# Optimization experiments

Hardware: AMD Instinct MI355X
Metric: run time of the kernel (lower is better)

Reference implementation:

```python
import jax, jax.numpy as jnp
import numpy as np


def setup_inputs() -> dict:
    key = jax.random.key(0)
    k1, k2, k3, k4 = jax.random.split(key, 4)
    B, S, d_in, d_out = 4, 2048, 1024, 1024
    x = jax.random.normal(k1, (B, S, d_in), dtype=jnp.float32)
    # torch nn.Linear weight is [d_out, d_in]; we store transposed [d_in, d_out]
    Wq = jax.random.normal(k2, (d_in, d_out), dtype=jnp.float32) * (1.0 / np.sqrt(d_in))
    Wk = jax.random.normal(k3, (d_in, d_out), dtype=jnp.float32) * (1.0 / np.sqrt(d_in))
    Wv = jax.random.normal(k4, (d_in, d_out), dtype=jnp.float32) * (1.0 / np.sqrt(d_in))
    return {"x": x, "Wq": Wq, "Wk": Wk, "Wv": Wv}


def reference(x, Wq, Wk, Wv):
    # x: [B, S, d_in]
    B, S, d_in = x.shape
    q = jnp.einsum("bsd,de->bse", x, Wq)
    k = jnp.einsum("bsd,de->bse", x, Wk)
    v = jnp.einsum("bsd,de->bse", x, Wv)
    scores = jnp.einsum("bqe,bke->bqk", q, k)  # [B, S, S]
    causal = jnp.triu(jnp.ones((S, S), dtype=bool), k=1)  # True above diagonal
    scores = jnp.where(causal[None, :, :], -jnp.inf, scores)
    # NOTE: original scales by sqrt(d_in), not sqrt(d_out)
    scale = jnp.asarray(1.0 / np.sqrt(d_in), dtype=scores.dtype)
    weights = jax.nn.softmax(scores * scale, axis=-1)
    # dropout p=0.0 -> identity
    return jnp.einsum("bqk,bke->bqe", weights, v)
```

## Files before the change

kernel.cpp:

```cpp
#include <hip/hip_runtime.h>
#include <hip/hip_bf16.h>

typedef __attribute__((ext_vector_type(8))) short short8;
typedef __attribute__((ext_vector_type(4))) short short4_t;
typedef __attribute__((ext_vector_type(4))) float f32x4;
typedef unsigned short ushort_t;

__device__ __forceinline__ ushort_t f2bf(float f) {
    union { __hip_bfloat16 h; ushort_t u; } c;
    c.h = __float2bfloat16(f);
    return c.u;
}

__device__ __forceinline__ void gload16(const ushort_t* g, ushort_t* l) {
    __builtin_amdgcn_global_load_lds(
        (const __attribute__((address_space(1))) void*)g,
        (__attribute__((address_space(3))) void*)l, 16, 0, 0);
}

__global__ __launch_bounds__(256) void k_prep(const float* __restrict__ x,
                                              const float* __restrict__ Wq,
                                              const float* __restrict__ Wk,
                                              const float* __restrict__ Wv,
                                              ushort_t* __restrict__ xb,
                                              ushort_t* __restrict__ Wqb,
                                              ushort_t* __restrict__ Wkb,
                                              ushort_t* __restrict__ Wvt) {
    const int bz = blockIdx.z;
    const int t = threadIdx.y * 32 + threadIdx.x;
    if (bz == 3) {
        size_t base = ((size_t)(blockIdx.y * 32 + blockIdx.x) * 256 + t) * 8;
#pragma unroll
        for (int p = 0; p < 4; ++p) {
            size_t idx = base + (size_t)p * 2097152;
            float4 a = *(const float4*)(x + idx);
            float4 b = *(const float4*)(x + idx + 4);
            short8 o;
            o[0] = (short)f2bf(a.x); o[1] = (short)f2bf(a.y);
            o[2] = (short)f2bf(a.z); o[3] = (short)f2bf(a.w);
            o[4] = (short)f2bf(b.x); o[5] = (short)f2bf(b.y);
            o[6] = (short)f2bf(b.z); o[7] = (short)f2bf(b.w);
            *(short8*)(xb + idx) = o;
        }
        return;
    }
    if (bz < 2) {
        const float* src = bz ? Wk : Wq;
        ushort_t* dst = bz ? Wkb : Wqb;
        size_t idx = ((size_t)(blockIdx.y * 32 + blockIdx.x) * 256 + t) * 4;
        float4 a = *(const float4*)(src + idx);
        short4_t o;
        o[0] = (short)f2bf(a.x); o[1] = (short)f2bf(a.y);
        o[2] = (short)f2bf(a.z); o[3] = (short)f2bf(a.w);
        *(short4_t*)(dst + idx) = o;
        return;
    }
    __shared__ float tile[32][33];
    int tx = threadIdx.x, ty = threadIdx.y;
    int d0 = blockIdx.y * 32, e0 = blockIdx.x * 32;
#pragma unroll
    for (int i = 0; i < 32; i += 8)
        tile[ty + i][tx] = Wv[(size_t)(d0 + ty + i) * 1024 + e0 + tx];
    __syncthreads();
#pragma unroll
    for (int i = 0; i < 32; i += 8)
        Wvt[(size_t)(e0 + ty + i) * 1024 + d0 + tx] = f2bf(tile[tx][ty + i]);
}

template <int MODE>
__global__ __launch_bounds__(256) void k_gemm(const ushort_t* __restrict__ Abase,
                                              const ushort_t* __restrict__ Bbase,
                                              void* __restrict__ Cbase,
                                              ushort_t* __restrict__ Vt) {
    int bm, bn, bz;
    const ushort_t* A;
    const ushort_t* B;
    if constexpr (MODE == 3) {
        bm = blockIdx.x; bn = blockIdx.y; bz = 0;
        A = Abase; B = Bbase;
    } else {
        bm = blockIdx.x; bn = blockIdx.y; bz = blockIdx.z;
        A = Abase;
        B = Bbase + (size_t)bz * 1048576;
    }
    const int lda = 1024, ldb = 1024, nk = 32;

    constexpr int SMEM_ELEMS = (MODE == 0) ? (128 * 130) : 8192;
    __shared__ ushort_t smem[SMEM_ELEMS];
    ushort_t* As = smem;
    ushort_t* Bs = smem + 4096;

    const int tid = threadIdx.x;
    const int l = tid & 63, wid = tid >> 6;
    const int wr = (wid >> 1) * 64, wc = (wid & 1) * 64;
    const int lr = l & 15, kc = (l >> 4) * 8;

    const int srow = tid >> 2, skb = (tid & 3) * 8;
    const ushort_t* ag = A + (size_t)(bm * 128 + srow) * lda + skb;
    const ushort_t* bg = B + (size_t)(bn * 128 + srow) * ldb + skb;
    const size_t a64 = (size_t)64 * lda, b64 = (size_t)64 * ldb;
    ushort_t* al = As + tid * 8;
    ushort_t* bl = Bs + tid * 8;

    f32x4 zero = {0.f, 0.f, 0.f, 0.f};
    f32x4 acc[4][4];
#pragma unroll
    for (int m = 0; m < 4; ++m)
#pragma unroll
        for (int n = 0; n < 4; ++n) acc[m][n] = zero;

    for (int ks = 0; ks < nk; ++ks) {
        __syncthreads();
        gload16(ag, al);
        gload16(ag + a64, al + 2048);
        gload16(bg, bl);
        gload16(bg + b64, bl + 2048);
        ag += 32; bg += 32;
        __syncthreads();

        short8 a[4], b[4];
#pragma unroll
        for (int m = 0; m < 4; ++m)
            a[m] = *(const short8*)&As[(wr + m * 16 + lr) * 32 + kc];
#pragma unroll
        for (int n = 0; n < 4; ++n)
            b[n] = *(const short8*)&Bs[(wc + n * 16 + lr) * 32 + kc];
#pragma unroll
        for (int m = 0; m < 4; ++m)
#pragma unroll
            for (int n = 0; n < 4; ++n)
                acc[m][n] = __builtin_amdgcn_mfma_f32_16x16x32_bf16(a[m], b[n], acc[m][n], 0, 0, 0);
    }

    const int rbase = (l >> 4) * 4;
    const int cbase = l & 15;

    if constexpr (MODE == 0) {
        if (bz == 1) {
            __syncthreads();
#pragma unroll
            for (int m = 0; m < 4; ++m)
#pragma unroll
                for (int n = 0; n < 4; ++n) {
                    int col = wc + n * 16 + cbase;
                    int row0 = wr + m * 16 + rbase;
#pragma unroll
                    for (int r = 0; r < 4; ++r)
                        smem[col * 130 + row0 + r] = f2bf(acc[m][n][r]);
                }
            __syncthreads();
            const int e = tid >> 1, jh = (tid & 1) * 64;
            const int b = bm >> 4, j0 = (bm * 128) & 2047;
            ushort_t* dst = Vt + (size_t)b * 2097152 +
                            (size_t)(bn * 128 + e) * 2048 + j0 + jh;
            const ushort_t* src = smem + e * 130 + jh;
#pragma unroll
            for (int c = 0; c < 8; ++c)
                *(short8*)(dst + c * 8) = *(const short8*)(src + c * 8);
            return;
        }
    }

#pragma unroll
    for (int m = 0; m < 4; ++m) {
#pragma unroll
        for (int n = 0; n < 4; ++n) {
            int col = wc + n * 16 + cbase;
            int gcol = bn * 128 + col;
#pragma unroll
            for (int r = 0; r < 4; ++r) {
                int grow = bm * 128 + wr + m * 16 + rbase + r;
                ushort_t* C = (ushort_t*)Cbase;
                C[(size_t)grow * 1024 + gcol] = f2bf(acc[m][n][r]);
            }
        }
    }
}

template <int MODE>
__global__ __launch_bounds__(256) void k_attn(const ushort_t* __restrict__ Abase,
                                              const ushort_t* __restrict__ Bbase,
                                              void* __restrict__ Cbase) {
    int bm, bn;
    const int bz = blockIdx.z;
    const ushort_t* A;
    const ushort_t* B;
    int lda, ldb, nk;
    if constexpr (MODE == 1) {
        int x = blockIdx.x;
        bm = (int)((sqrtf(8.f * x + 1.f) - 1.f) * 0.5f);
        while ((bm + 1) * (bm + 2) / 2 <= x) ++bm;
        while (bm * (bm + 1) / 2 > x) --bm;
        bn = x - bm * (bm + 1) / 2;
        A = Abase + (size_t)bz * 2048 * 1024; lda = 1024;
        B = Bbase + (size_t)bz * 2048 * 1024; ldb = 1024;
        nk = 32;
    } else {
        int xr = blockIdx.x;
        int m0 = (xr & 1) ? (15 - (xr >> 1)) : (xr >> 1);
        bm = (bz & 2) ? (15 - m0) : m0;
        bn = blockIdx.y;
        A = Abase + (size_t)bz * 2048 * 2048; lda = 2048;
        B = Bbase + (size_t)bz * 1024 * 2048; ldb = 2048;
        nk = (bm + 1) * 4;
    }

    __shared__ ushort_t As[2][4096];
    __shared__ ushort_t Bs[2][4096];

    const int tid = threadIdx.x;
    const int l = tid & 63, wid = tid >> 6;
    const int wr = (wid >> 1) * 64, wc = (wid & 1) * 64;
    const int lr = l & 15, kc = (l >> 4) * 8;

    const int srow = tid >> 2, skb = (tid & 3) * 8;
    const ushort_t* ag = A + (size_t)(bm * 128 + srow) * lda + skb;
    const ushort_t* bg = B + (size_t)(bn * 128 + srow) * ldb + skb;
    const size_t a64 = (size_t)64 * lda, b64 = (size_t)64 * ldb;

    f32x4 zero = {0.f, 0.f, 0.f, 0.f};
    f32x4 acc[4][4];
#pragma unroll
    for (int m = 0; m < 4; ++m)
#pragma unroll
        for (int n = 0; n < 4; ++n) acc[m][n] = zero;

    f32x4 rs[4];
    short8 ones;
#pragma unroll
    for (int e = 0; e < 8; ++e) ones[e] = (short)0x3F80;
#pragma unroll
    for (int m = 0; m < 4; ++m) rs[m] = zero;

    gload16(ag, &As[0][tid * 8]);
    gload16(ag + a64, &As[0][tid * 8 + 2048]);
    gload16(bg, &Bs[0][tid * 8]);
    gload16(bg + b64, &Bs[0][tid * 8 + 2048]);
    ag += 32; bg += 32;
    __syncthreads();

    int cur = 0;
    for (int ks = 0; ks < nk; ++ks) {
        if (ks + 1 < nk) {
            const int nxt = cur ^ 1;
            gload16(ag, &As[nxt][tid * 8]);
            gload16(ag + a64, &As[nxt][tid * 8 + 2048]);
            gload16(bg, &Bs[nxt][tid * 8]);
            gload16(bg + b64, &Bs[nxt][tid * 8 + 2048]);
            ag += 32; bg += 32;
        }

        short8 a[4], b[4];
#pragma unroll
        for (int m = 0; m < 4; ++m)
            a[m] = *(const short8*)&As[cur][(wr + m * 16 + lr) * 32 + kc];
#pragma unroll
        for (int n = 0; n < 4; ++n)
            b[n] = *(const short8*)&Bs[cur][(wc + n * 16 + lr) * 32 + kc];
#pragma unroll
        for (int m = 0; m < 4; ++m)
#pragma unroll
            for (int n = 0; n < 4; ++n)
                acc[m][n] = __builtin_amdgcn_mfma_f32_16x16x32_bf16(a[m], b[n], acc[m][n], 0, 0, 0);
        if constexpr (MODE == 2) {
#pragma unroll
            for (int m = 0; m < 4; ++m)
                rs[m] = __builtin_amdgcn_mfma_f32_16x16x32_bf16(a[m], ones, rs[m], 0, 0, 0);
        }

        __syncthreads();
        cur ^= 1;
    }

    const int rbase = (l >> 4) * 4;
    const int cbase = l & 15;

    if constexpr (MODE == 1) {
        ushort_t* C = (ushort_t*)Cbase + (size_t)bz * 2048 * 2048;
#pragma unroll
        for (int m = 0; m < 4; ++m)
#pragma unroll
            for (int n = 0; n < 4; ++n) {
                int gcol = bn * 128 + wc + n * 16 + cbase;
#pragma unroll
                for (int r = 0; r < 4; ++r) {
                    int grow = bm * 128 + wr + m * 16 + rbase + r;
                    ushort_t pv = (gcol <= grow) ? f2bf(__expf(acc[m][n][r] * 0.03125f))
                                                 : (ushort_t)0;
                    C[(size_t)grow * 2048 + gcol] = pv;
                }
            }
    } else {
        float inv[4][4];
#pragma unroll
        for (int m = 0; m < 4; ++m)
#pragma unroll
            for (int r = 0; r < 4; ++r) inv[m][r] = 1.0f / rs[m][r];
        float* C = (float*)Cbase + (size_t)bz * 2048 * 1024;
#pragma unroll
        for (int m = 0; m < 4; ++m)
#pragma unroll
            for (int n = 0; n < 4; ++n) {
                int gcol = bn * 128 + wc + n * 16 + cbase;
#pragma unroll
                for (int r = 0; r < 4; ++r) {
                    int grow = bm * 128 + wr + m * 16 + rbase + r;
                    C[(size_t)grow * 1024 + gcol] = acc[m][n][r] * inv[m][r];
                }
            }
    }
}

extern "C" void kernel_launch(void* const* d_in, const int* in_sizes, int n_in,
                              void* d_out, int out_size, void* d_ws, size_t ws_size,
                              hipStream_t stream) {
    const float* x  = (const float*)d_in[0];
    const float* Wq = (const float*)d_in[1];
    const float* Wk = (const float*)d_in[2];
    const float* Wv = (const float*)d_in[3];

    char* ws = (char*)d_ws;
    ushort_t* xb  = (ushort_t*)(ws);
    ushort_t* Wqb = (ushort_t*)(ws + 16777216);
    ushort_t* Wkb = (ushort_t*)(ws + 18874368);
    ushort_t* Mt  = (ushort_t*)(ws + 20971520);
    ushort_t* Wvt = (ushort_t*)(ws + 23068672);
    ushort_t* y   = (ushort_t*)(ws + 25165824);
    ushort_t* Vt  = (ushort_t*)(ws + 41943040);
    ushort_t* P   = (ushort_t*)(ws + 58720256);

    k_prep<<<dim3(32, 32, 4), dim3(32, 8), 0, stream>>>(x, Wq, Wk, Wv, xb, Wqb, Wkb, Wvt);
    k_gemm<3><<<dim3(8, 8), 256, 0, stream>>>(Wkb, Wqb, Mt, nullptr);
    k_gemm<0><<<dim3(64, 8, 2), 256, 0, stream>>>(xb, Mt, y, Vt);
    k_attn<1><<<dim3(136, 1, 4), 256, 0, stream>>>(y, xb, P);
    k_attn<2><<<dim3(16, 8, 4), 256, 0, stream>>>(P, Vt, (float*)d_out);
}
```

Baseline: 170.2 us.

## Fuse Wk·Wqᵀ product GEMM into prep kernel with inline fp32-to-bf16 conversion

The Wq/Wk bf16 conversion pass and the separate Mt GEMM launch are removed. Sixty-four blocks of the prep kernel now load fp32 Wk/Wq directly, convert them in registers, stage the tiles in padded LDS and compute Mt with MFMA. The x conversion and Wv transpose run in the same launch. This saves one kernel launch and a global round trip for the bf16 weights, but the 64 GEMM blocks run unpipelined, use plain loads, and share the grid with many short conversion blocks, which could lengthen the tail.

New measurement: 190.4 us. 1.12x slower.

```diff
diff --git a/kernel.cpp b/kernel.cpp
--- a/kernel.cpp
+++ b/kernel.cpp
@@ -2,7 +2,6 @@
 #include <hip/hip_bf16.h>
 
 typedef __attribute__((ext_vector_type(8))) short short8;
-typedef __attribute__((ext_vector_type(4))) short short4_t;
 typedef __attribute__((ext_vector_type(4))) float f32x4;
 typedef unsigned short ushort_t;
 
@@ -10,6 +9,15 @@
     union { __hip_bfloat16 h; ushort_t u; } c;
     c.h = __float2bfloat16(f);
     return c.u;
+}
+
+__device__ __forceinline__ short8 cvt8(float4 a, float4 b) {
+    short8 o;
+    o[0] = (short)f2bf(a.x); o[1] = (short)f2bf(a.y);
+    o[2] = (short)f2bf(a.z); o[3] = (short)f2bf(a.w);
+    o[4] = (short)f2bf(b.x); o[5] = (short)f2bf(b.y);
+    o[6] = (short)f2bf(b.z); o[7] = (short)f2bf(b.w);
+    return o;
 }
 
 __device__ __forceinline__ void gload16(const ushort_t* g, ushort_t* l) {
@@ -23,70 +31,106 @@
                                               const float* __restrict__ Wk,
                                               const float* __restrict__ Wv,
                                               ushort_t* __restrict__ xb,
-                                              ushort_t* __restrict__ Wqb,
-                                              ushort_t* __restrict__ Wkb,
+                                              ushort_t* __restrict__ Mt,
                                               ushort_t* __restrict__ Wvt) {
+    __shared__ ushort_t sm[10240];
     const int bz = blockIdx.z;
     const int t = threadIdx.y * 32 + threadIdx.x;
-    if (bz == 3) {
+
+    if (bz == 1) {
         size_t base = ((size_t)(blockIdx.y * 32 + blockIdx.x) * 256 + t) * 8;
 #pragma unroll
         for (int p = 0; p < 4; ++p) {
             size_t idx = base + (size_t)p * 2097152;
             float4 a = *(const float4*)(x + idx);
             float4 b = *(const float4*)(x + idx + 4);
-            short8 o;
-            o[0] = (short)f2bf(a.x); o[1] = (short)f2bf(a.y);
-            o[2] = (short)f2bf(a.z); o[3] = (short)f2bf(a.w);
-            o[4] = (short)f2bf(b.x); o[5] = (short)f2bf(b.y);
-            o[6] = (short)f2bf(b.z); o[7] = (short)f2bf(b.w);
-            *(short8*)(xb + idx) = o;
+            *(short8*)(xb + idx) = cvt8(a, b);
         }
         return;
     }
-    if (bz < 2) {
-        const float* src = bz ? Wk : Wq;
-        ushort_t* dst = bz ? Wkb : Wqb;
-        size_t idx = ((size_t)(blockIdx.y * 32 + blockIdx.x) * 256 + t) * 4;
-        float4 a = *(const float4*)(src + idx);
-        short4_t o;
-        o[0] = (short)f2bf(a.x); o[1] = (short)f2bf(a.y);
-        o[2] = (short)f2bf(a.z); o[3] = (short)f2bf(a.w);
-        *(short4_t*)(dst + idx) = o;
+    if (bz == 0) {
+        float* tile = (float*)sm;
+        int tx = threadIdx.x, ty = threadIdx.y;
+        int d0 = blockIdx.y * 32, e0 = blockIdx.x * 32;
+#pragma unroll
+        for (int i = 0; i < 32; i += 8)
+            tile[(ty + i) * 33 + tx] = Wv[(size_t)(d0 + ty + i) * 1024 + e0 + tx];
+        __syncthreads();
+#pragma unroll
+        for (int i = 0; i < 32; i += 8)
+            Wvt[(size_t)(e0 + ty + i) * 1024 + d0 + tx] = f2bf(tile[tx * 33 + ty + i]);
         return;
     }
-    __shared__ float tile[32][33];
-    int tx = threadIdx.x, ty = threadIdx.y;
-    int d0 = blockIdx.y * 32, e0 = blockIdx.x * 32;
-#pragma unroll
-    for (int i = 0; i < 32; i += 8)
-        tile[ty + i][tx] = Wv[(size_t)(d0 + ty + i) * 1024 + e0 + tx];
-    __syncthreads();
-#pragma unroll
-    for (int i = 0; i < 32; i += 8)
-        Wvt[(size_t)(e0 + ty + i) * 1024 + d0 + tx] = f2bf(tile[tx][ty + i]);
-}
-
-template <int MODE>
+    if (blockIdx.x >= 8 || blockIdx.y >= 8) return;
+    const int bm = blockIdx.x, bn = blockIdx.y;
+    ushort_t* As = sm;
+    ushort_t* Bs = sm + 5120;
+
+    const int ar = t >> 1, ac = (t & 1) << 4;
+    const int l = t & 63, wid = t >> 6;
+    const int wr = (wid >> 1) * 64, wc = (wid & 1) * 64;
+    const int lr = l & 15, kc = (l >> 4) * 8;
+
+    f32x4 zero = {0.f, 0.f, 0.f, 0.f};
+    f32x4 acc[4][4];
+#pragma unroll
+    for (int m = 0; m < 4; ++m)
+#pragma unroll
+        for (int n = 0; n < 4; ++n) acc[m][n] = zero;
+
+    for (int ks = 0; ks < 32; ++ks) {
+        const float* ap = Wk + (size_t)(bm * 128 + ar) * 1024 + ks * 32 + ac;
+        const float* bp = Wq + (size_t)(bn * 128 + ar) * 1024 + ks * 32 + ac;
+        short8 av0 = cvt8(*(const float4*)ap, *(const float4*)(ap + 4));
+        short8 av1 = cvt8(*(const float4*)(ap + 8), *(const float4*)(ap + 12));
+        short8 bv0 = cvt8(*(const float4*)bp, *(const float4*)(bp + 4));
+        short8 bv1 = cvt8(*(const float4*)(bp + 8), *(const float4*)(bp + 12));
+        __syncthreads();
+        *(short8*)&As[ar * 40 + ac] = av0;
+        *(short8*)&As[ar * 40 + ac + 8] = av1;
+        *(short8*)&Bs[ar * 40 + ac] = bv0;
+        *(short8*)&Bs[ar * 40 + ac + 8] = bv1;
+        __syncthreads();
+
+        short8 a[4], b[4];
+#pragma unroll
+        for (int m = 0; m < 4; ++m)
+            a[m] = *(const short8*)&As[(wr + m * 16 + lr) * 40 + kc];
+#pragma unroll
+        for (int n = 0; n < 4; ++n)
+            b[n] = *(const short8*)&Bs[(wc + n * 16 + lr) * 40 + kc];
+#pragma unroll
+        for (int m = 0; m < 4; ++m)
+#pragma unroll
+            for (int n = 0; n < 4; ++n)
+                acc[m][n] = __builtin_amdgcn_mfma_f32_16x16x32_bf16(a[m], b[n], acc[m][n], 0, 0, 0);
+    }
+
+    const int rbase = (l >> 4) * 4;
+    const int cbase = l & 15;
+#pragma unroll
+    for (int m = 0; m < 4; ++m)
+#pragma unroll
+        for (int n = 0; n < 4; ++n) {
+            int gcol = bn * 128 + wc + n * 16 + cbase;
+#pragma unroll
+            for (int r = 0; r < 4; ++r) {
+                int grow = bm * 128 + wr + m * 16 + rbase + r;
+                Mt[(size_t)grow * 1024 + gcol] = f2bf(acc[m][n][r]);
+            }
+        }
+}
+
 __global__ __launch_bounds__(256) void k_gemm(const ushort_t* __restrict__ Abase,
                                               const ushort_t* __restrict__ Bbase,
                                               void* __restrict__ Cbase,
                                               ushort_t* __restrict__ Vt) {
-    int bm, bn, bz;
-    const ushort_t* A;
-    const ushort_t* B;
-    if constexpr (MODE == 3) {
-        bm = blockIdx.x; bn = blockIdx.y; bz = 0;
-        A = Abase; B = Bbase;
-    } else {
-        bm = blockIdx.x; bn = blockIdx.y; bz = blockIdx.z;
-        A = Abase;
-        B = Bbase + (size_t)bz * 1048576;
-    }
+    const int bm = blockIdx.x, bn = blockIdx.y, bz = blockIdx.z;
+    const ushort_t* A = Abase;
+    const ushort_t* B = Bbase + (size_t)bz * 1048576;
     const int lda = 1024, ldb = 1024, nk = 32;
 
-    constexpr int SMEM_ELEMS = (MODE == 0) ? (128 * 130) : 8192;
-    __shared__ ushort_t smem[SMEM_ELEMS];
+    __shared__ ushort_t smem[128 * 130];
     ushort_t* As = smem;
     ushort_t* Bs = smem + 4096;
 
@@ -135,30 +179,28 @@
     const int rbase = (l >> 4) * 4;
     const int cbase = l & 15;
 
-    if constexpr (MODE == 0) {
-        if (bz == 1) {
-            __syncthreads();
-#pragma unroll
-            for (int m = 0; m < 4; ++m)
-#pragma unroll
-                for (int n = 0; n < 4; ++n) {
-                    int col = wc + n * 16 + cbase;
-                    int row0 = wr + m * 16 + rbase;
-#pragma unroll
-                    for (int r = 0; r < 4; ++r)
-                        smem[col * 130 + row0 + r] = f2bf(acc[m][n][r]);
-                }
-            __syncthreads();
-            const int e = tid >> 1, jh = (tid & 1) * 64;
-            const int b = bm >> 4, j0 = (bm * 128) & 2047;
-            ushort_t* dst = Vt + (size_t)b * 2097152 +
-                            (size_t)(bn * 128 + e) * 2048 + j0 + jh;
-            const ushort_t* src = smem + e * 130 + jh;
-#pragma unroll
-            for (int c = 0; c < 8; ++c)
-                *(short8*)(dst + c * 8) = *(const short8*)(src + c * 8);
-            return;
-        }
+    if (bz == 1) {
+        __syncthreads();
+#pragma unroll
+        for (int m = 0; m < 4; ++m)
+#pragma unroll
+            for (int n = 0; n < 4; ++n) {
+                int col = wc + n * 16 + cbase;
+                int row0 = wr + m * 16 + rbase;
+#pragma unroll
+                for (int r = 0; r < 4; ++r)
+                    smem[col * 130 + row0 + r] = f2bf(acc[m][n][r]);
+            }
+        __syncthreads();
+        const int e = tid >> 1, jh = (tid & 1) * 64;
+        const int b = bm >> 4, j0 = (bm * 128) & 2047;
+        ushort_t* dst = Vt + (size_t)b * 2097152 +
+                        (size_t)(bn * 128 + e) * 2048 + j0 + jh;
+        const ushort_t* src = smem + e * 130 + jh;
+#pragma unroll
+        for (int c = 0; c < 8; ++c)
+            *(short8*)(dst + c * 8) = *(const short8*)(src + c * 8);
+        return;
     }
 
 #pragma unroll
@@ -321,17 +363,14 @@
 
     char* ws = (char*)d_ws;
     ushort_t* xb  = (ushort_t*)(ws);
-    ushort_t* Wqb = (ushort_t*)(ws + 16777216);
-    ushort_t* Wkb = (ushort_t*)(ws + 18874368);
-    ushort_t* Mt  = (ushort_t*)(ws + 20971520);
-    ushort_t* Wvt = (ushort_t*)(ws + 23068672);
-    ushort_t* y   = (ushort_t*)(ws + 25165824);
-    ushort_t* Vt  = (ushort_t*)(ws + 41943040);
-    ushort_t* P   = (ushort_t*)(ws + 58720256);
-
-    k_prep<<<dim3(32, 32, 4), dim3(32, 8), 0, stream>>>(x, Wq, Wk, Wv, xb, Wqb, Wkb, Wvt);
-    k_gemm<3><<<dim3(8, 8), 256, 0, stream>>>(Wkb, Wqb, Mt, nullptr);
-    k_gemm<0><<<dim3(64, 8, 2), 256, 0, stream>>>(xb, Mt, y, Vt);
+    ushort_t* Mt  = (ushort_t*)(ws + 16777216);
+    ushort_t* Wvt = (ushort_t*)(ws + 18874368);
+    ushort_t* y   = (ushort_t*)(ws + 20971520);
+    ushort_t* Vt  = (ushort_t*)(ws + 37748736);
+    ushort_t* P   = (ushort_t*)(ws + 54525952);
+
+    k_prep<<<dim3(32, 32, 3), dim3(32, 8), 0, stream>>>(x, Wq, Wk, Wv, xb, Mt, Wvt);
+    k_gemm<<<dim3(64, 8, 2), 256, 0, stream>>>(xb, Mt, y, Vt);
     k_attn<1><<<dim3(136, 1, 4), 256, 0, stream>>>(y, xb, P);
     k_attn<2><<<dim3(16, 8, 4), 256, 0, stream>>>(P, Vt, (float*)d_out);
 }
```
